# Performance work log

Hardware: AMD Instinct MI355X
Metric: run time of the kernel (lower is better)

## Reference

```python
import jax, jax.numpy as jnp
import numpy as np

E = 1024
H = 16
D = E // H  # 64
SCALE = float(D ** 0.5)  # module MULTIPLIES by sqrt(d_head), faithful to source


def setup_inputs() -> dict:
    key = jax.random.key(0)
    k1, k2, k3 = jax.random.split(key, 3)
    x = jax.random.normal(k1, (4, 2048, E), dtype=jnp.float32)
    # store weights as [in, out] so forward is x @ W (equiv to torch Linear with W.T)
    w_qkv = jax.random.normal(k2, (E, 3 * E), dtype=jnp.float32) * (1.0 / np.sqrt(E))
    w_out = jax.random.normal(k3, (E, E), dtype=jnp.float32) * (1.0 / np.sqrt(E))
    return {"x": x, "w_qkv": w_qkv, "w_out": w_out}


def reference(x, w_qkv, w_out):
    b, t, _ = x.shape
    qkv = x @ w_qkv  # [b, t, 3E]
    # einops 'b t (d k h) -> k b h t d' with k=3, h=H: innermost axis is h
    qkv = qkv.reshape(b, t, D, 3, H)
    qkv = jnp.transpose(qkv, (3, 0, 4, 1, 2))  # [3, b, h, t, d]
    q, k, v = qkv[0], qkv[1], qkv[2]
    energy = jnp.einsum('bhid,bhjd->bhij', q, k) * SCALE  # note: multiply, per source
    attn = jax.nn.softmax(energy, axis=-1)
    o = jnp.einsum('bhij,bhjd->bhid', attn, v)
    o = jnp.transpose(o, (0, 2, 1, 3)).reshape(b, t, H * D)  # 'b h t d -> b t (h d)'
    return o @ w_out
```

## Files before the change

kernel.cpp:

```cpp
#include <hip/hip_runtime.h>

typedef __attribute__((ext_vector_type(4))) float f32x4;
typedef __attribute__((ext_vector_type(16))) float f32x16;
typedef __attribute__((ext_vector_type(8))) short bf16x8;
typedef __attribute__((ext_vector_type(4))) unsigned short u16x4;

#define NB 4
#define NT 2048
#define NE 1024
#define NH 16
#define ND 64
#define NM (NB*NT)

__device__ inline unsigned short f2bf(float f){
  unsigned int u = __float_as_uint(f);
  return (unsigned short)((u + 0x7fffu + ((u >> 16) & 1u)) >> 16);
}
__device__ inline float bf2f(unsigned short s){
  return __uint_as_float(((unsigned int)s) << 16);
}
__device__ inline unsigned short f2h(float f){
  union { _Float16 h; unsigned short u; } c;
  c.h = (_Float16)f;
  return c.u;
}
__device__ inline float h2f(unsigned short s){
  union { _Float16 h; unsigned short u; } c;
  c.u = s;
  return (float)c.h;
}
__device__ inline f32x4 mfma16(bf16x8 a, bf16x8 b, f32x4 c){
  return __builtin_amdgcn_mfma_f32_16x16x32_bf16(a, b, c, 0, 0, 0);
}
__device__ inline f32x16 mfma32h(bf16x8 a, bf16x8 b, f32x16 c){
  return __builtin_amdgcn_mfma_f32_32x32x16_f16(a, b, c, 0, 0, 0);
}
__device__ inline void gload_lds16(const unsigned short* g, unsigned short* l){
  __builtin_amdgcn_global_load_lds(
      (const __attribute__((address_space(1))) void*)g,
      (__attribute__((address_space(3))) void*)l, 16, 0, 0);
}
__device__ inline float max3f(float a, float b, float c){
  float r;
  asm("v_max3_f32 %0, %1, %2, %3" : "=v"(r) : "v"(a), "v"(b), "v"(c));
  return r;
}

__global__ __launch_bounds__(256) void prep_x_k(const float* __restrict__ x,
    unsigned short* __restrict__ xh, unsigned short* __restrict__ xl, int n4){
  int stride = gridDim.x * 256;
  for (int i = blockIdx.x * 256 + threadIdx.x; i < n4; i += stride){
    f32x4 v = ((const f32x4*)x)[i];
    u16x4 hi, lo;
    #pragma unroll
    for (int j = 0; j < 4; j++){
      hi[j] = f2bf(v[j]);
      lo[j] = f2bf(v[j] - bf2f(hi[j]));
    }
    ((u16x4*)xh)[i] = hi;
    ((u16x4*)xl)[i] = lo;
  }
}

__global__ __launch_bounds__(256) void prep_wq_k(const float* __restrict__ w,
    unsigned short* __restrict__ wh, unsigned short* __restrict__ wl){
  __shared__ float tile[32][33];
  int tx = threadIdx.x & 31, ty = threadIdx.x >> 5;
  int c0 = blockIdx.x * 32, k0 = blockIdx.y * 32;
  #pragma unroll
  for (int i = 0; i < 32; i += 8)
    tile[ty + i][tx] = w[(size_t)(k0 + ty + i) * 3072 + c0 + tx];
  __syncthreads();
  #pragma unroll
  for (int i = 0; i < 32; i += 8){
    int col = c0 + ty + i;
    int d = col / 48, r = col % 48;
    int kk = r >> 4, h = r & 15;
    int n = kk * 1024 + h * 64 + d;
    float v = tile[tx][ty + i];
    unsigned short hi = f2bf(v);
    wh[(size_t)n * NE + k0 + tx] = hi;
    wl[(size_t)n * NE + k0 + tx] = f2bf(v - bf2f(hi));
  }
}

__global__ __launch_bounds__(256) void prep_wo_k(const float* __restrict__ w,
    unsigned short* __restrict__ wt){
  __shared__ float tile[32][33];
  int tx = threadIdx.x & 31, ty = threadIdx.x >> 5;
  int n0 = blockIdx.x * 32, k0 = blockIdx.y * 32;
  #pragma unroll
  for (int i = 0; i < 32; i += 8)
    tile[ty + i][tx] = w[(size_t)(k0 + ty + i) * NE + n0 + tx];
  __syncthreads();
  #pragma unroll
  for (int i = 0; i < 32; i += 8)
    wt[(size_t)(n0 + ty + i) * NE + k0 + tx] = f2bf(tile[tx][ty + i]);
}

template<int SPLIT, int EPI>
__global__ __launch_bounds__(256) void gemm_k(
    const unsigned short* __restrict__ Ah, const unsigned short* __restrict__ Al,
    const unsigned short* __restrict__ Bh, const unsigned short* __restrict__ Bl,
    float* __restrict__ Cf,
    unsigned short* __restrict__ Qh, unsigned short* __restrict__ Ql,
    unsigned short* __restrict__ Kh, unsigned short* __restrict__ Kl,
    unsigned short* __restrict__ Vt,
    int M, int N, int K){
  __shared__ unsigned short lds[SPLIT ? 4 : 2][128 * 32];
  const int tid = threadIdx.x;
  const int w = tid >> 6, l = tid & 63;
  const int wr = w >> 1, wc = w & 1;
  const int m0 = blockIdx.y * 128, n0 = blockIdx.x * 128;

  f32x4 acc[4][4];
  #pragma unroll
  for (int i = 0; i < 4; i++)
    #pragma unroll
    for (int j = 0; j < 4; j++) acc[i][j] = (f32x4){0.f, 0.f, 0.f, 0.f};

  const int lr = l >> 2;
  const int lkb = (l & 3) * 8;

  for (int k0 = 0; k0 < K; k0 += 32){
    #pragma unroll
    for (int cc = 0; cc < 2; cc++){
      int c = w + cc * 4;
      size_t ga = (size_t)(m0 + c * 16 + lr) * K + k0 + lkb;
      size_t gb = (size_t)(n0 + c * 16 + lr) * K + k0 + lkb;
      gload_lds16(Ah + ga, &lds[0][c * 512]);
      gload_lds16(Bh + gb, &lds[1][c * 512]);
      if (SPLIT){
        gload_lds16(Al + ga, &lds[2][c * 512]);
        gload_lds16(Bl + gb, &lds[3][c * 512]);
      }
    }
    __syncthreads();
    bf16x8 ah[4], bh_[4], al[4], bl_[4];
    #pragma unroll
    for (int mi = 0; mi < 4; mi++){
      int o = (wr * 64 + mi * 16 + (l & 15)) * 32 + (l >> 4) * 8;
      ah[mi] = *(bf16x8*)&lds[0][o];
      if (SPLIT) al[mi] = *(bf16x8*)&lds[2][o];
    }
    #pragma unroll
    for (int ni = 0; ni < 4; ni++){
      int o = (wc * 64 + ni * 16 + (l & 15)) * 32 + (l >> 4) * 8;
      bh_[ni] = *(bf16x8*)&lds[1][o];
      if (SPLIT) bl_[ni] = *(bf16x8*)&lds[3][o];
    }
    #pragma unroll
    for (int mi = 0; mi < 4; mi++)
      #pragma unroll
      for (int ni = 0; ni < 4; ni++){
        acc[mi][ni] = mfma16(ah[mi], bh_[ni], acc[mi][ni]);
        if (SPLIT){
          acc[mi][ni] = mfma16(ah[mi], bl_[ni], acc[mi][ni]);
          acc[mi][ni] = mfma16(al[mi], bh_[ni], acc[mi][ni]);
        }
      }
    __syncthreads();
  }

  #pragma unroll
  for (int mi = 0; mi < 4; mi++){
    #pragma unroll
    for (int ni = 0; ni < 4; ni++){
      #pragma unroll
      for (int j = 0; j < 4; j++){
        int row = m0 + wr * 64 + mi * 16 + (l >> 4) * 4 + j;
        int col = n0 + wc * 64 + ni * 16 + (l & 15);
        float v = acc[mi][ni][j];
        if (EPI == 0){
          Cf[(size_t)row * N + col] = v;
        } else if (EPI == 1){
          int kk = col >> 10, h = (col >> 6) & 15, d = col & 63;
          int bb = row >> 11, t = row & (NT - 1);
          size_t off = ((size_t)(bb * NH + h) * NT + t) * ND + d;
          if (kk == 0){
            Qh[off] = f2h(v);
          } else {
            unsigned short hi = f2h(v);
            Kh[off] = hi; Kl[off] = f2h(v - h2f(hi));
          }
        } else {
          int h = col >> 6, d = col & 63;
          int bb = row >> 11, t = row & (NT - 1);
          Vt[((size_t)(bb * NH + h) * ND + d) * NT + t] = f2h(v);
        }
      }
    }
  }
}

__global__ __launch_bounds__(256, 3) void attn_k(
    const unsigned short* __restrict__ Qh,
    const unsigned short* __restrict__ Kh, const unsigned short* __restrict__ Kl,
    const unsigned short* __restrict__ Vt, unsigned short* __restrict__ O){
  __shared__ unsigned short kh_lds[2][64 * 64];
  __shared__ unsigned short kl_lds[2][64 * 64];
  __shared__ unsigned short vt_lds[2][64 * 64];
  const int tid = threadIdx.x;
  const int w = tid >> 6, l = tid & 63;
  const int qi = l & 31, hi = l >> 5;
  const int bid = blockIdx.x;
  const int xcd = bid & 7, slot = bid >> 3;
  const int bh_i = xcd + 8 * (slot >> 4);
  const int qt = slot & 15;
  const int b = bh_i >> 4, h = bh_i & 15;
  const int i0 = qt * 128 + w * 32;
  const size_t bh = (size_t)bh_i;

  const unsigned short* KhG = Kh + bh * NT * ND;
  const unsigned short* KlG = Kl + bh * NT * ND;
  const unsigned short* VtG = Vt + bh * ND * NT;

  bf16x8 qh[4];
  {
    const unsigned short* qb = Qh + (bh * NT + i0 + qi) * ND + hi * 8;
    #pragma unroll
    for (int c = 0; c < 4; c++) qh[c] = *(const bf16x8*)(qb + c * 16);
  }

  f32x16 o0, o1;
  #pragma unroll
  for (int r = 0; r < 16; r++){ o0[r] = 0.f; o1[r] = 0.f; }
  float mrun = -3.0e38f, lrun = 0.f;

  const int rk = l >> 3;
  const int ck = (l & 7) ^ rk;

  auto STAGE = [&](int buf, int j0){
    gload_lds16(KhG + (size_t)(j0 + 16 * w + rk) * ND + ck * 8,     &kh_lds[buf][(16 * w) * 64]);
    gload_lds16(KhG + (size_t)(j0 + 16 * w + 8 + rk) * ND + ck * 8, &kh_lds[buf][(16 * w + 8) * 64]);
    gload_lds16(KlG + (size_t)(j0 + 16 * w + rk) * ND + ck * 8,     &kl_lds[buf][(16 * w) * 64]);
    gload_lds16(KlG + (size_t)(j0 + 16 * w + 8 + rk) * ND + ck * 8, &kl_lds[buf][(16 * w + 8) * 64]);
    gload_lds16(VtG + (size_t)(16 * w + rk) * NT + j0 + ck * 8,     &vt_lds[buf][(16 * w) * 64]);
    gload_lds16(VtG + (size_t)(16 * w + 8 + rk) * NT + j0 + ck * 8, &vt_lds[buf][(16 * w + 8) * 64]);
  };

  auto STEP = [&](int buf, int half){
    const char* KH = (const char*)&kh_lds[buf][0];
    const char* KL = (const char*)&kl_lds[buf][0];
    const char* VT = (const char*)&vt_lds[buf][0];
    bf16x8 kh[4], kl[4];
    #pragma unroll
    for (int c = 0; c < 4; c++){
      int off = (half * 32 + qi) * 128 + (((2 * c + hi) ^ (qi & 7)) * 16);
      kh[c] = *(const bf16x8*)(KH + off);
      kl[c] = *(const bf16x8*)(KL + off);
    }

    f32x16 t1, t2;
    #pragma unroll
    for (int r = 0; r < 16; r++){ t1[r] = 0.f; t2[r] = 0.f; }
    __builtin_amdgcn_s_setprio(1);
    #pragma unroll
    for (int c = 0; c < 4; c++){
      t1 = mfma32h(kh[c], qh[c], t1);
      t2 = mfma32h(kl[c], qh[c], t2);
    }
    __builtin_amdgcn_s_setprio(0);
    f32x16 s = t1 + t2;

    bf16x8 vb[2][2];
    #pragma unroll
    for (int dt = 0; dt < 2; dt++)
      #pragma unroll
      for (int k0 = 0; k0 < 2; k0++){
        int off = (dt * 32 + qi) * 128 + (((half * 4 + 2 * k0 + hi) ^ (qi & 7)) * 16);
        vb[dt][k0] = *(const bf16x8*)(VT + off);
      }

    float m1 = max3f(s[0], s[1], s[2]);
    float m2 = max3f(s[3], s[4], s[5]);
    float m3 = max3f(s[6], s[7], s[8]);
    float m4 = max3f(s[9], s[10], s[11]);
    float m5 = max3f(s[12], s[13], s[14]);
    float pm = fmaxf(max3f(m1, m2, m3), max3f(m4, m5, s[15]));
    pm = fmaxf(pm, __shfl_xor(pm, 32));
    float Lm = pm * 8.0f;
    if (!__all(Lm <= mrun + 8.0f)){
      float nm = fmaxf(mrun, Lm);
      float sc = __expf(mrun - nm);
      mrun = nm;
      lrun *= sc;
      #pragma unroll
      for (int r = 0; r < 16; r++){
        int mrow = (r & 3) + 8 * (r >> 2) + 4 * hi;
        float scr = __shfl(sc, mrow);
        o0[r] *= scr;
        o1[r] *= scr;
      }
    }
    float p[16];
    #pragma unroll
    for (int r = 0; r < 16; r++) p[r] = __expf(fmaf(s[r], 8.0f, -mrun));
    float u8[8], u4[4];
    #pragma unroll
    for (int i = 0; i < 8; i++) u8[i] = p[2 * i] + p[2 * i + 1];
    #pragma unroll
    for (int i = 0; i < 4; i++) u4[i] = u8[2 * i] + u8[2 * i + 1];
    float rs = (u4[0] + u4[1]) + (u4[2] + u4[3]);
    rs += __shfl_xor(rs, 32);
    lrun += rs;

    unsigned int pk[8];
    #pragma unroll
    for (int i = 0; i < 8; i++)
      asm("v_cvt_pkrtz_f16_f32 %0, %1, %2" : "=v"(pk[i]) : "v"(p[2 * i]), "v"(p[2 * i + 1]));
    unsigned int sw[8];
    #pragma unroll
    for (int i = 0; i < 8; i++) sw[i] = __shfl_xor(pk[i], 32);

    union { unsigned int u[4]; bf16x8 v; } pa0, pa1;
    pa0.u[0] = hi ? sw[2] : pk[0];
    pa0.u[1] = hi ? sw[3] : pk[1];
    pa0.u[2] = hi ? pk[2] : sw[0];
    pa0.u[3] = hi ? pk[3] : sw[1];
    pa1.u[0] = hi ? sw[6] : pk[4];
    pa1.u[1] = hi ? sw[7] : pk[5];
    pa1.u[2] = hi ? pk[6] : sw[4];
    pa1.u[3] = hi ? pk[7] : sw[5];

    __builtin_amdgcn_s_setprio(1);
    o0 = mfma32h(pa0.v, vb[0][0], o0);
    o0 = mfma32h(pa1.v, vb[0][1], o0);
    o1 = mfma32h(pa0.v, vb[1][0], o1);
    o1 = mfma32h(pa1.v, vb[1][1], o1);
    __builtin_amdgcn_s_setprio(0);
  };

  STAGE(0, 0);
  asm volatile("s_waitcnt vmcnt(0)" ::: "memory");
  __syncthreads();
  int buf = 0;
  for (int j0 = 0; j0 < NT; j0 += 64){
    if (j0 + 64 < NT) STAGE(buf ^ 1, j0 + 64);
    STEP(buf, 0);
    STEP(buf, 1);
    __syncthreads();
    buf ^= 1;
  }

  float rl = 1.0f / lrun;
  #pragma unroll
  for (int r = 0; r < 16; r++){
    int mrow = (r & 3) + 8 * (r >> 2) + 4 * hi;
    float f = __shfl(rl, mrow);
    size_t base = ((size_t)b * NT + i0 + mrow) * NE + h * ND + qi;
    O[base]      = f2bf(o0[r] * f);
    O[base + 32] = f2bf(o1[r] * f);
  }
}

extern "C" void kernel_launch(void* const* d_in, const int* in_sizes, int n_in,
                              void* d_out, int out_size, void* d_ws, size_t ws_size,
                              hipStream_t stream){
  const float* x     = (const float*)d_in[0];
  const float* w_qkv = (const float*)d_in[1];
  const float* w_out = (const float*)d_in[2];
  float* out = (float*)d_out;

  char* ws = (char*)d_ws;
  const size_t SZ_X  = (size_t)NM * NE * 2;
  const size_t SZ_WQ = (size_t)3072 * NE * 2;
  const size_t SZ_WO = (size_t)NE * NE * 2;
  const size_t SZ_T  = (size_t)NB * NH * NT * ND * 2;

  unsigned short* xh  = (unsigned short*)(ws);
  unsigned short* xl  = (unsigned short*)(ws + SZ_X);
  unsigned short* wqh = (unsigned short*)(ws + 2 * SZ_X);
  unsigned short* wql = (unsigned short*)(ws + 2 * SZ_X + SZ_WQ);
  unsigned short* wto = (unsigned short*)(ws + 2 * SZ_X + 2 * SZ_WQ);
  unsigned short* Qh  = (unsigned short*)(ws + 2 * SZ_X + 2 * SZ_WQ + SZ_WO);
  unsigned short* Ql  = Qh + (SZ_T / 2);
  unsigned short* Kh  = Qh + 2 * (SZ_T / 2);
  unsigned short* Kl  = Qh + 3 * (SZ_T / 2);
  unsigned short* Vt   = xl;
  unsigned short* Obuf = xh;

  const size_t NEED = 2 * SZ_X + 2 * SZ_WQ + SZ_WO + 4 * SZ_T;
  if (ws_size < NEED) return;

  prep_x_k<<<2048, 256, 0, stream>>>(x, xh, xl, NM * NE / 4);
  prep_wq_k<<<dim3(3072 / 32, 1024 / 32), 256, 0, stream>>>(w_qkv, wqh, wql);
  prep_wo_k<<<dim3(1024 / 32, 1024 / 32), 256, 0, stream>>>(w_out, wto);
  gemm_k<1, 1><<<dim3(2048 / 128, NM / 128), 256, 0, stream>>>(
      xh, xl, wqh, wql, nullptr, Qh, Ql, Kh, Kl, nullptr, NM, 2048, NE);
  gemm_k<0, 2><<<dim3(1024 / 128, NM / 128), 256, 0, stream>>>(
      xh, nullptr, wqh + (size_t)2048 * NE, nullptr, nullptr,
      nullptr, nullptr, nullptr, nullptr, Vt, NM, 1024, NE);
  attn_k<<<dim3(1024), 256, 0, stream>>>(Qh, Kh, Kl, Vt, Obuf);
  gemm_k<0, 0><<<dim3(NE / 128, NM / 128), 256, 0, stream>>>(
      Obuf, nullptr, wto, nullptr, out,
      nullptr, nullptr, nullptr, nullptr, nullptr, NM, NE, NE);
}
```

Baseline: 356.0 us.

## Replace split-bf16 QKV GEMM with single fp16 GEMM and merge V projection

The QKV projection previously used a hi/lo bf16 split (three MFMAs per tile) for Q and K, plus a separate GEMM for V. Now x and w_qkv are converted once to fp16 and a single fp16 MFMA GEMM covers all 3072 output columns, routing V to its transposed layout in the epilogue. This removes the extra low-part conversions, the extra loads and two-thirds of the QK-projection MFMAs, and one kernel launch. In exchange the projection runs at plain fp16 precision, with a risk of accuracy loss or overflow if activations are large, since the scaled-up logits amplify errors.

```diff
diff --git a/kernel.cpp b/kernel.cpp
--- a/kernel.cpp
+++ b/kernel.cpp
@@ -29,8 +29,11 @@
   c.u = s;
   return (float)c.h;
 }
-__device__ inline f32x4 mfma16(bf16x8 a, bf16x8 b, f32x4 c){
+__device__ inline f32x4 mfma16b(bf16x8 a, bf16x8 b, f32x4 c){
   return __builtin_amdgcn_mfma_f32_16x16x32_bf16(a, b, c, 0, 0, 0);
+}
+__device__ inline f32x4 mfma16h(bf16x8 a, bf16x8 b, f32x4 c){
+  return __builtin_amdgcn_mfma_f32_16x16x32_f16(a, b, c, 0, 0, 0);
 }
 __device__ inline f32x16 mfma32h(bf16x8 a, bf16x8 b, f32x16 c){
   return __builtin_amdgcn_mfma_f32_32x32x16_f16(a, b, c, 0, 0, 0);
@@ -47,23 +50,19 @@
 }
 
 __global__ __launch_bounds__(256) void prep_x_k(const float* __restrict__ x,
-    unsigned short* __restrict__ xh, unsigned short* __restrict__ xl, int n4){
+    unsigned short* __restrict__ xh, int n4){
   int stride = gridDim.x * 256;
   for (int i = blockIdx.x * 256 + threadIdx.x; i < n4; i += stride){
     f32x4 v = ((const f32x4*)x)[i];
-    u16x4 hi, lo;
-    #pragma unroll
-    for (int j = 0; j < 4; j++){
-      hi[j] = f2bf(v[j]);
-      lo[j] = f2bf(v[j] - bf2f(hi[j]));
-    }
-    ((u16x4*)xh)[i] = hi;
-    ((u16x4*)xl)[i] = lo;
+    u16x4 o;
+    #pragma unroll
+    for (int j = 0; j < 4; j++) o[j] = f2h(v[j]);
+    ((u16x4*)xh)[i] = o;
   }
 }
 
 __global__ __launch_bounds__(256) void prep_wq_k(const float* __restrict__ w,
-    unsigned short* __restrict__ wh, unsigned short* __restrict__ wl){
+    unsigned short* __restrict__ wq){
   __shared__ float tile[32][33];
   int tx = threadIdx.x & 31, ty = threadIdx.x >> 5;
   int c0 = blockIdx.x * 32, k0 = blockIdx.y * 32;
@@ -77,10 +76,7 @@
     int d = col / 48, r = col % 48;
     int kk = r >> 4, h = r & 15;
     int n = kk * 1024 + h * 64 + d;
-    float v = tile[tx][ty + i];
-    unsigned short hi = f2bf(v);
-    wh[(size_t)n * NE + k0 + tx] = hi;
-    wl[(size_t)n * NE + k0 + tx] = f2bf(v - bf2f(hi));
+    wq[(size_t)n * NE + k0 + tx] = f2h(tile[tx][ty + i]);
   }
 }
 
@@ -98,16 +94,16 @@
     wt[(size_t)(n0 + ty + i) * NE + k0 + tx] = f2bf(tile[tx][ty + i]);
 }
 
-template<int SPLIT, int EPI>
+template<int EPI>
 __global__ __launch_bounds__(256) void gemm_k(
-    const unsigned short* __restrict__ Ah, const unsigned short* __restrict__ Al,
-    const unsigned short* __restrict__ Bh, const unsigned short* __restrict__ Bl,
+    const unsigned short* __restrict__ A,
+    const unsigned short* __restrict__ Bt,
     float* __restrict__ Cf,
-    unsigned short* __restrict__ Qh, unsigned short* __restrict__ Ql,
+    unsigned short* __restrict__ Qh,
     unsigned short* __restrict__ Kh, unsigned short* __restrict__ Kl,
     unsigned short* __restrict__ Vt,
     int M, int N, int K){
-  __shared__ unsigned short lds[SPLIT ? 4 : 2][128 * 32];
+  __shared__ unsigned short lds[2][128 * 32];
   const int tid = threadIdx.x;
   const int w = tid >> 6, l = tid & 63;
   const int wr = w >> 1, wc = w & 1;
@@ -126,39 +122,23 @@
     #pragma unroll
     for (int cc = 0; cc < 2; cc++){
       int c = w + cc * 4;
-      size_t ga = (size_t)(m0 + c * 16 + lr) * K + k0 + lkb;
-      size_t gb = (size_t)(n0 + c * 16 + lr) * K + k0 + lkb;
-      gload_lds16(Ah + ga, &lds[0][c * 512]);
-      gload_lds16(Bh + gb, &lds[1][c * 512]);
-      if (SPLIT){
-        gload_lds16(Al + ga, &lds[2][c * 512]);
-        gload_lds16(Bl + gb, &lds[3][c * 512]);
-      }
+      gload_lds16(A  + (size_t)(m0 + c * 16 + lr) * K + k0 + lkb, &lds[0][c * 512]);
+      gload_lds16(Bt + (size_t)(n0 + c * 16 + lr) * K + k0 + lkb, &lds[1][c * 512]);
     }
     __syncthreads();
-    bf16x8 ah[4], bh_[4], al[4], bl_[4];
-    #pragma unroll
-    for (int mi = 0; mi < 4; mi++){
-      int o = (wr * 64 + mi * 16 + (l & 15)) * 32 + (l >> 4) * 8;
-      ah[mi] = *(bf16x8*)&lds[0][o];
-      if (SPLIT) al[mi] = *(bf16x8*)&lds[2][o];
-    }
-    #pragma unroll
-    for (int ni = 0; ni < 4; ni++){
-      int o = (wc * 64 + ni * 16 + (l & 15)) * 32 + (l >> 4) * 8;
-      bh_[ni] = *(bf16x8*)&lds[1][o];
-      if (SPLIT) bl_[ni] = *(bf16x8*)&lds[3][o];
-    }
+    bf16x8 af[4], bfr[4];
+    #pragma unroll
+    for (int mi = 0; mi < 4; mi++)
+      af[mi] = *(bf16x8*)&lds[0][(wr * 64 + mi * 16 + (l & 15)) * 32 + (l >> 4) * 8];
+    #pragma unroll
+    for (int ni = 0; ni < 4; ni++)
+      bfr[ni] = *(bf16x8*)&lds[1][(wc * 64 + ni * 16 + (l & 15)) * 32 + (l >> 4) * 8];
     #pragma unroll
     for (int mi = 0; mi < 4; mi++)
       #pragma unroll
-      for (int ni = 0; ni < 4; ni++){
-        acc[mi][ni] = mfma16(ah[mi], bh_[ni], acc[mi][ni]);
-        if (SPLIT){
-          acc[mi][ni] = mfma16(ah[mi], bl_[ni], acc[mi][ni]);
-          acc[mi][ni] = mfma16(al[mi], bh_[ni], acc[mi][ni]);
-        }
-      }
+      for (int ni = 0; ni < 4; ni++)
+        acc[mi][ni] = EPI ? mfma16h(af[mi], bfr[ni], acc[mi][ni])
+                          : mfma16b(af[mi], bfr[ni], acc[mi][ni]);
     __syncthreads();
   }
 
@@ -173,20 +153,20 @@
         float v = acc[mi][ni][j];
         if (EPI == 0){
           Cf[(size_t)row * N + col] = v;
-        } else if (EPI == 1){
+        } else {
           int kk = col >> 10, h = (col >> 6) & 15, d = col & 63;
           int bb = row >> 11, t = row & (NT - 1);
-          size_t off = ((size_t)(bb * NH + h) * NT + t) * ND + d;
-          if (kk == 0){
-            Qh[off] = f2h(v);
+          if (kk == 2){
+            Vt[((size_t)(bb * NH + h) * ND + d) * NT + t] = f2h(v);
           } else {
-            unsigned short hi = f2h(v);
-            Kh[off] = hi; Kl[off] = f2h(v - h2f(hi));
+            size_t off = ((size_t)(bb * NH + h) * NT + t) * ND + d;
+            if (kk == 0){
+              Qh[off] = f2h(v);
+            } else {
+              unsigned short hi = f2h(v);
+              Kh[off] = hi; Kl[off] = f2h(v - h2f(hi));
+            }
           }
-        } else {
-          int h = col >> 6, d = col & 63;
-          int bb = row >> 11, t = row & (NT - 1);
-          Vt[((size_t)(bb * NH + h) * ND + d) * NT + t] = f2h(v);
         }
       }
     }
@@ -369,30 +349,23 @@
   const size_t SZ_T  = (size_t)NB * NH * NT * ND * 2;
 
   unsigned short* xh  = (unsigned short*)(ws);
-  unsigned short* xl  = (unsigned short*)(ws + SZ_X);
-  unsigned short* wqh = (unsigned short*)(ws + 2 * SZ_X);
-  unsigned short* wql = (unsigned short*)(ws + 2 * SZ_X + SZ_WQ);
-  unsigned short* wto = (unsigned short*)(ws + 2 * SZ_X + 2 * SZ_WQ);
-  unsigned short* Qh  = (unsigned short*)(ws + 2 * SZ_X + 2 * SZ_WQ + SZ_WO);
-  unsigned short* Ql  = Qh + (SZ_T / 2);
-  unsigned short* Kh  = Qh + 2 * (SZ_T / 2);
-  unsigned short* Kl  = Qh + 3 * (SZ_T / 2);
-  unsigned short* Vt   = xl;
+  unsigned short* wq  = (unsigned short*)(ws + SZ_X);
+  unsigned short* wto = (unsigned short*)(ws + SZ_X + SZ_WQ);
+  unsigned short* Qh  = (unsigned short*)(ws + SZ_X + SZ_WQ + SZ_WO);
+  unsigned short* Kh  = Qh + (SZ_T / 2);
+  unsigned short* Kl  = Qh + 2 * (SZ_T / 2);
+  unsigned short* Vt  = Qh + 3 * (SZ_T / 2);
   unsigned short* Obuf = xh;
 
-  const size_t NEED = 2 * SZ_X + 2 * SZ_WQ + SZ_WO + 4 * SZ_T;
+  const size_t NEED = SZ_X + SZ_WQ + SZ_WO + 4 * SZ_T;
   if (ws_size < NEED) return;
 
-  prep_x_k<<<2048, 256, 0, stream>>>(x, xh, xl, NM * NE / 4);
-  prep_wq_k<<<dim3(3072 / 32, 1024 / 32), 256, 0, stream>>>(w_qkv, wqh, wql);
+  prep_x_k<<<2048, 256, 0, stream>>>(x, xh, NM * NE / 4);
+  prep_wq_k<<<dim3(3072 / 32, 1024 / 32), 256, 0, stream>>>(w_qkv, wq);
   prep_wo_k<<<dim3(1024 / 32, 1024 / 32), 256, 0, stream>>>(w_out, wto);
-  gemm_k<1, 1><<<dim3(2048 / 128, NM / 128), 256, 0, stream>>>(
-      xh, xl, wqh, wql, nullptr, Qh, Ql, Kh, Kl, nullptr, NM, 2048, NE);
-  gemm_k<0, 2><<<dim3(1024 / 128, NM / 128), 256, 0, stream>>>(
-      xh, nullptr, wqh + (size_t)2048 * NE, nullptr, nullptr,
-      nullptr, nullptr, nullptr, nullptr, Vt, NM, 1024, NE);
+  gemm_k<1><<<dim3(3072 / 128, NM / 128), 256, 0, stream>>>(
+      xh, wq, nullptr, Qh, Kh, Kl, Vt, NM, 3072, NE);
   attn_k<<<dim3(1024), 256, 0, stream>>>(Qh, Kh, Kl, Vt, Obuf);
-  gemm_k<0, 0><<<dim3(NE / 128, NM / 128), 256, 0, stream>>>(
-      Obuf, nullptr, wto, nullptr, out,
-      nullptr, nullptr, nullptr, nullptr, nullptr, NM, NE, NE);
-}
+  gemm_k<0><<<dim3(NE / 128, NM / 128), 256, 0, stream>>>(
+      Obuf, wto, out, nullptr, nullptr, nullptr, nullptr, NM, NE, NE);
+}
```

Result: faster. 304.5 us (median of 2 runs) (-14.5%).
